# Performance work log

Measured on AMD Instinct MI355X. Metric: run time of the kernel, lower is better.

## Reference

```python
import math
import jax, jax.numpy as jnp
import numpy as np

B, T, D = 2, 2048, 1024
NUM_HEADS = 16
NUM_KV_HEADS = 4
HEAD_DIM = 64
ROPE_THETA = 500000.0


def precompute_freqs_cis(dim, seq_len, theta):
    freqs = 1.0 / theta ** (jnp.arange(0, dim, 2).astype(jnp.float32) / dim)
    freqs = jnp.outer(jnp.arange(seq_len), freqs)  # [T, dim//2]
    return jnp.cos(freqs), jnp.sin(freqs)


def apply_rotary_emb(xq, xk, cos, sin):
    # xq:[B,T,H,Dh], cos/sin:[T,Dh//2] -> broadcast as [1,T,1,Dh//2]
    c = cos[None, :, None, :]
    s = sin[None, :, None, :]

    def rot(x):
        xr = x.reshape(*x.shape[:-1], -1, 2)
        x0, x1 = xr[..., 0], xr[..., 1]
        return jnp.stack([x0 * c - x1 * s, x1 * c + x0 * s], axis=-1).reshape(x.shape)

    return rot(xq), rot(xk)


def setup_inputs() -> dict:
    key = jax.random.key(0)
    ks = jax.random.split(key, 5)
    x = jax.random.normal(ks[0], (B, T, D), dtype=jnp.float32)
    # causal mask [B,1,T,T]
    mask = jnp.broadcast_to(jnp.tril(jnp.ones((T, T), dtype=bool))[None, None], (B, 1, T, T))
    sq = 1.0 / math.sqrt(D)
    Wq = jax.random.normal(ks[1], (D, NUM_HEADS * HEAD_DIM), dtype=jnp.float32) * sq
    Wk = jax.random.normal(ks[2], (D, NUM_KV_HEADS * HEAD_DIM), dtype=jnp.float32) * sq
    Wv = jax.random.normal(ks[3], (D, NUM_KV_HEADS * HEAD_DIM), dtype=jnp.float32) * sq
    Wo = jax.random.normal(ks[4], (NUM_HEADS * HEAD_DIM, D), dtype=jnp.float32) * (1.0 / math.sqrt(NUM_HEADS * HEAD_DIM))
    return {"x": x, "mask": mask, "Wq": Wq, "Wk": Wk, "Wv": Wv, "Wo": Wo}


def reference(x, mask, Wq, Wk, Wv, Wo):
    b, t, _ = x.shape
    n_rep = NUM_HEADS // NUM_KV_HEADS
    q = (x @ Wq).reshape(b, t, NUM_HEADS, HEAD_DIM)
    k = (x @ Wk).reshape(b, t, NUM_KV_HEADS, HEAD_DIM)
    v = (x @ Wv).reshape(b, t, NUM_KV_HEADS, HEAD_DIM)
    cos, sin = precompute_freqs_cis(HEAD_DIM, t, ROPE_THETA)
    q, k = apply_rotary_emb(q, k, cos, sin)
    k = jnp.repeat(k, n_rep, axis=2)
    v = jnp.repeat(v, n_rep, axis=2)
    q = q.transpose(0, 2, 1, 3)  # [B,H,T,Dh]
    k = k.transpose(0, 2, 1, 3)
    v = v.transpose(0, 2, 1, 3)
    scale = 1.0 / math.sqrt(HEAD_DIM)
    attn = jnp.einsum('bhqd,bhkd->bhqk', q, k) * scale
    attn = jnp.where(mask, attn, -1e9)
    attn = jax.nn.softmax(attn, axis=-1)
    out = jnp.einsum('bhqk,bhkd->bhqd', attn, v)
    out = out.transpose(0, 2, 1, 3).reshape(b, t, -1)
    return out @ Wo
```

## Files before the change

kernel.cpp:

```cpp
#include <hip/hip_runtime.h>
#include <hip/hip_bf16.h>

#define B_  2
#define T_  2048
#define D_  1024
#define H_  16
#define KH_ 4
#define DH_ 64

typedef __attribute__((ext_vector_type(8))) short bf16x8;
typedef __attribute__((ext_vector_type(4))) float f32x4;

#define QSCALE 0.18033688011112043f

#if defined(__has_builtin)
#  if __has_builtin(__builtin_amdgcn_exp2f)
#    define EXP2F(x) __builtin_amdgcn_exp2f(x)
#  endif
#endif
#ifndef EXP2F
#  define EXP2F(x) exp2f(x)
#endif

__device__ __forceinline__ unsigned short f2bf(float f) {
  union { float f; unsigned int u; } v; v.f = f;
  return (unsigned short)((v.u + 0x7FFFu + ((v.u >> 16) & 1u)) >> 16);
}
__device__ __forceinline__ unsigned int pk2(float a, float b) {
  union { __hip_bfloat162 h2; unsigned int u; } v;
  v.h2 = __float22bfloat162_rn(make_float2(a, b));
  return v.u;
}

__device__ __forceinline__ void g2l16(const void* g, void* l) {
  __builtin_amdgcn_global_load_lds(
      (const __attribute__((address_space(1))) void*)g,
      (__attribute__((address_space(3))) void*)l, 16, 0, 0);
}


__global__ __launch_bounds__(256) void prep_kernel(
    const float* __restrict__ x,  const float* __restrict__ Wq,
    const float* __restrict__ Wk, const float* __restrict__ Wv,
    const float* __restrict__ Wo,
    short* __restrict__ xb, short* __restrict__ WT, short* __restrict__ WoT,
    float2* __restrict__ tbl) {
  __shared__ short Ts[64 * 72];
  const int bid = blockIdx.x, tid = threadIdx.x;

  if (bid < 2048) {
    const size_t i8 = ((size_t)bid * 256 + tid) * 8;
    const float4 a = *(const float4*)&x[i8];
    const float4 b = *(const float4*)&x[i8 + 4];
    uint4 p; p.x = pk2(a.x, a.y); p.y = pk2(a.z, a.w);
    p.z = pk2(b.x, b.y); p.w = pk2(b.z, b.w);
    *(uint4*)&xb[i8] = p;
  } else if (bid < 2688) {
    const bool isW = bid < 2432;
    const int idx = isW ? (bid - 2048) : (bid - 2432);
    const int n0 = (idx >> 4) * 64, k0 = (idx & 15) * 64;
    const float* src; int ncols, c0; short* dst;
    if (isW) {
      dst = WT;
      if (n0 < 1024)      { src = Wq; ncols = 1024; c0 = n0; }
      else if (n0 < 1280) { src = Wk; ncols = 256;  c0 = n0 - 1024; }
      else                { src = Wv; ncols = 256;  c0 = n0 - 1280; }
    } else { dst = WoT; src = Wo; ncols = 1024; c0 = n0; }
    for (int i = tid; i < 1024; i += 256) {
      const int kr = i >> 4, c4 = (i & 15) << 2;
      const int kc = isW ? kr : ((kr & 15) * 4 + (kr >> 4));
      const float4 w = *(const float4*)&src[(size_t)(k0 + kr) * ncols + c0 + c4];
      Ts[(c4 + 0) * 72 + kc] = (short)f2bf(w.x);
      Ts[(c4 + 1) * 72 + kc] = (short)f2bf(w.y);
      Ts[(c4 + 2) * 72 + kc] = (short)f2bf(w.z);
      Ts[(c4 + 3) * 72 + kc] = (short)f2bf(w.w);
    }
    __syncthreads();
    for (int c = tid; c < 512; c += 256) {
      const int nr = c >> 3, c8 = (c & 7) * 8;
      *(bf16x8*)&dst[(size_t)(n0 + nr) * 1024 + k0 + c8] =
          *(const bf16x8*)&Ts[nr * 72 + c8];
    }
  } else {
    const int e = (bid - 2688) * 256 + tid;
    const int t = e >> 5, i2 = e & 31;
    const float freq = exp2f(-(float)(2 * i2) * (18.931568569324174f / 64.0f));
    float sn, cs; sincosf((float)t * freq, &sn, &cs);
    tbl[e] = make_float2(cs, sn);
  }
}

__global__ __launch_bounds__(256) void qkv_mfma_kernel(
    const short* __restrict__ xb, const short* __restrict__ WT,
    const float2* __restrict__ tbl,
    short* __restrict__ qo, short* __restrict__ ko, short* __restrict__ vt) {
  __shared__ short Xsh[2][128 * 64];
  __shared__ short Wth[2][64 * 64];
  const int tid = threadIdx.x;
  const int lane = tid & 63, w = tid >> 6;
  const int lm = lane & 15, quad = lane >> 4;
  const int bid = blockIdx.x;
  const int xcd = bid & 7, slot = bid >> 3;
  const int m0 = (xcd * 4 + (slot & 3)) * 128;
  const int n0 = (slot >> 2) * 64;

  f32x4 acc[2][4];
  #pragma unroll
  for (int sm = 0; sm < 2; ++sm)
    #pragma unroll
    for (int ct = 0; ct < 4; ++ct) acc[sm][ct] = (f32x4){0.f, 0.f, 0.f, 0.f};

  auto stage = [&](int kt, int bsel) {
    #pragma unroll
    for (int u = 0; u < 4; ++u) {
      const int r = u * 32 + w * 8 + (lane >> 3);
      const int sb = (lane & 7) ^ (r & 7);
      g2l16(&xb[(size_t)(m0 + r) * 1024 + kt * 64 + sb * 8],
            &Xsh[bsel][(u * 32 + w * 8) * 64]);
    }
    #pragma unroll
    for (int u = 0; u < 2; ++u) {
      const int r = u * 32 + w * 8 + (lane >> 3);
      const int sb = (lane & 7) ^ (r & 7);
      g2l16(&WT[(size_t)(n0 + r) * 1024 + kt * 64 + sb * 8],
            &Wth[bsel][(u * 32 + w * 8) * 64]);
    }
  };

  stage(0, 0);
  for (int kt = 0; kt < 16; ++kt) {
    const int bsel = kt & 1;
    if (kt < 15) {
      stage(kt + 1, bsel ^ 1);
      asm volatile("s_waitcnt vmcnt(6)" ::: "memory");
    } else {
      asm volatile("s_waitcnt vmcnt(0)" ::: "memory");
    }
    __builtin_amdgcn_s_barrier();
    __builtin_amdgcn_sched_barrier(0);
    #pragma unroll
    for (int s2 = 0; s2 < 2; ++s2) {
      bf16x8 bfr[4];
      #pragma unroll
      for (int ct = 0; ct < 4; ++ct)
        bfr[ct] = *(const bf16x8*)&Wth[bsel][(ct * 16 + lm) * 64 +
                                            (((s2 * 4 + quad) ^ (lm & 7)) << 3)];
      #pragma unroll
      for (int sm = 0; sm < 2; ++sm) {
        const bf16x8 a = *(const bf16x8*)&Xsh[bsel][(w * 32 + sm * 16 + lm) * 64 +
                                            (((s2 * 4 + quad) ^ (lm & 7)) << 3)];
        #pragma unroll
        for (int ct = 0; ct < 4; ++ct)
          acc[sm][ct] =
              __builtin_amdgcn_mfma_f32_16x16x32_bf16(a, bfr[ct], acc[sm][ct], 0, 0, 0);
      }
    }
    __builtin_amdgcn_sched_barrier(0);
    __builtin_amdgcn_s_barrier();
  }

  if (n0 < 1280) {
    const bool isQ = n0 < 1024;
    short* outp = isQ ? qo : ko;
    const int base = isQ ? n0 : n0 - 1024;
    const int nh = isQ ? H_ : KH_;
    const int hh = base >> 6;
    const float post = isQ ? QSCALE : 1.0f;
    #pragma unroll
    for (int sm = 0; sm < 2; ++sm)
      #pragma unroll
      for (int r = 0; r < 4; ++r) {
        const int row = m0 + w * 32 + sm * 16 + quad * 4 + r;
        const int b = row >> 11, t = row & 2047;
        float v4[4];
        #pragma unroll
        for (int ct = 0; ct < 4; ++ct) {
          float val = acc[sm][ct][r];
          const float other = __shfl_xor(val, 1);
          const int ci = ct * 16 + lm;
          const float2 cs = tbl[t * 32 + (ci >> 1)];
          val = ((ci & 1) == 0) ? (val * cs.x - other * cs.y)
                                : (val * cs.x + other * cs.y);
          v4[ct] = val * post;
        }
        uint2 st; st.x = pk2(v4[0], v4[1]); st.y = pk2(v4[2], v4[3]);
        *(uint2*)&outp[((size_t)(b * nh + hh) * T_ + t) * DH_ + lm * 4] = st;
      }
  } else {
    short* XsF = &Xsh[0][0];
    __syncthreads();
    #pragma unroll
    for (int sm = 0; sm < 2; ++sm)
      #pragma unroll
      for (int r = 0; r < 4; ++r)
        #pragma unroll
        for (int ct = 0; ct < 4; ++ct)
          XsF[(w * 32 + sm * 16 + quad * 4 + r) * 72 + ct * 16 + lm] =
              (short)f2bf(acc[sm][ct][r]);
    __syncthreads();
    const int kh = (n0 - 1280) >> 6;
    const int b = m0 >> 11, t0 = m0 & 2047;
    short* vb = vt + (size_t)(b * KH_ + kh) * DH_ * T_;
    for (int c = tid; c < 1024; c += 256) {
      const int d = c >> 4, c8 = (c & 15) * 8;
      short tmp[8];
      #pragma unroll
      for (int j = 0; j < 8; ++j) {
        const int s = c8 + j, sg = s & 63;
        const int tok = (s & 64) | (sg & 35) | (((sg >> 2) & 1) << 4) |
                        (((sg >> 3) & 3) << 2);
        tmp[j] = XsF[tok * 72 + d];
      }
      *(bf16x8*)&vb[(size_t)d * T_ + t0 + c8] = *(bf16x8*)tmp;
    }
  }
}

__global__ __launch_bounds__(256, 4) void attn_mfma_kernel(
    const short* __restrict__ q, const short* __restrict__ k,
    const short* __restrict__ vt, short* __restrict__ att) {
  __shared__ short Ks[128 * 72];
  __shared__ short Vts[64 * 136];

  const int bx = blockIdx.x;
  const int jj = bx & 255, c2 = bx >> 8;
  int qt = (c2 & 1) ? (jj >> 3) : (31 - (jj >> 3));
  const int hb = (jj & 7) | (c2 << 3);
  const int h = hb >> 1, b = hb & 1;
  const int kh = h >> 2;
  const int tid = threadIdx.x;
  const int lane = tid & 63, w = tid >> 6;
  const int lm = lane & 15, quad = lane >> 4;
  const int q0 = qt * 64;

  const short* qb = q + (size_t)(b * H_ + h) * T_ * DH_;
  const short* kb = k + (size_t)(b * KH_ + kh) * T_ * DH_;
  const short* vb = vt + (size_t)(b * KH_ + kh) * DH_ * T_;

  bf16x8 ones;
  #pragma unroll
  for (int i = 0; i < 8; ++i) ones[i] = (short)0x3F80;

  bf16x8 aq[2];
  #pragma unroll
  for (int s = 0; s < 2; ++s)
    aq[s] = *(const bf16x8*)&qb[(size_t)(q0 + w * 16 + lm) * 64 + s * 32 + quad * 8];

  bf16x8 pk[4], pv[4];
  #pragma unroll
  for (int u = 0; u < 4; ++u) {
    const int c = tid + u * 256;
    const int row = c >> 3, c8 = (c & 7) * 8;
    pk[u] = *(const bf16x8*)&kb[(size_t)row * 64 + c8];
    const int d = c >> 4, c16 = (c & 15) * 8;
    pv[u] = *(const bf16x8*)&vb[(size_t)d * T_ + c16];
  }

  f32x4 oacc[4], lacc;
  #pragma unroll
  for (int i = 0; i < 4; ++i) oacc[i] = (f32x4){0.f, 0.f, 0.f, 0.f};
  lacc = (f32x4){0.f, 0.f, 0.f, 0.f};

  auto step = [&](int j, bool diag) {
    f32x4 sacc[4];
    #pragma unroll
    for (int i = 0; i < 4; ++i) sacc[i] = (f32x4){0.f, 0.f, 0.f, 0.f};
    __builtin_amdgcn_s_setprio(1);
    #pragma unroll
    for (int s2 = 0; s2 < 2; ++s2) {
      #pragma unroll
      for (int ct = 0; ct < 4; ++ct) {
        if (diag && ct > w) continue;
        const bf16x8 bb =
            *(const bf16x8*)&Ks[(j * 64 + ct * 16 + lm) * 72 + s2 * 32 + quad * 8];
        sacc[ct] = __builtin_amdgcn_mfma_f32_16x16x32_bf16(bb, aq[s2], sacc[ct], 0, 0, 0);
      }
    }
    __builtin_amdgcn_s_setprio(0);
    unsigned int pd[4][2];
    #pragma unroll
    for (int ct = 0; ct < 4; ++ct) {
      float p[4];
      #pragma unroll
      for (int r = 0; r < 4; ++r) {
        float e;
        if (diag && ct > w) e = 0.f;
        else {
          e = EXP2F(sacc[ct][r]);
          if (diag && ct == w && (quad * 4 + r) > lm) e = 0.f;
        }
        p[r] = e;
      }
      pd[ct][0] = pk2(p[0], p[1]);
      pd[ct][1] = pk2(p[2], p[3]);
    }
    __builtin_amdgcn_s_setprio(1);
    #pragma unroll
    for (int s2 = 0; s2 < 2; ++s2) {
      if (diag && 2 * s2 > w) continue;
      union { bf16x8 v; unsigned int u[4]; } pa;
      pa.u[0] = pd[2 * s2][0];     pa.u[1] = pd[2 * s2][1];
      pa.u[2] = pd[2 * s2 + 1][0]; pa.u[3] = pd[2 * s2 + 1][1];
      lacc = __builtin_amdgcn_mfma_f32_16x16x32_bf16(pa.v, ones, lacc, 0, 0, 0);
      #pragma unroll
      for (int ct = 0; ct < 4; ++ct) {
        const bf16x8 vfr = *(const bf16x8*)&Vts[(ct * 16 + lm) * 136 +
                                                j * 64 + s2 * 32 + quad * 8];
        oacc[ct] = __builtin_amdgcn_mfma_f32_16x16x32_bf16(pa.v, vfr, oacc[ct], 0, 0, 0);
      }
    }
    __builtin_amdgcn_s_setprio(0);
  };

  auto stage = [&](int r2) {
    __syncthreads();
    #pragma unroll
    for (int u = 0; u < 4; ++u) {
      const int c = tid + u * 256;
      const int row = c >> 3, c8 = (c & 7) * 8;
      *(bf16x8*)&Ks[row * 72 + c8] = pk[u];
      const int d = c >> 4, c16 = (c & 15) * 8;
      *(bf16x8*)&Vts[d * 136 + c16] = pv[u];
    }
    __syncthreads();
    const int r2n = (r2 + 2 <= qt) ? (r2 + 2) : r2;
    #pragma unroll
    for (int u = 0; u < 4; ++u) {
      const int c = tid + u * 256;
      const int row = c >> 3, c8 = (c & 7) * 8;
      pk[u] = *(const bf16x8*)&kb[(size_t)(r2n * 64 + row) * 64 + c8];
      const int d = c >> 4, c16 = (c & 15) * 8;
      pv[u] = *(const bf16x8*)&vb[(size_t)d * T_ + r2n * 64 + c16];
    }
  };

  int r2 = 0;
  for (; r2 + 1 <= qt; r2 += 2) {
    stage(r2);
    step(0, false);
    step(1, r2 + 1 == qt);
  }
  if (r2 == qt) {
    stage(r2);
    step(0, true);
  }

  #pragma unroll
  for (int r = 0; r < 4; ++r) {
    const int qrow = q0 + w * 16 + quad * 4 + r;
    const float inv = 1.f / lacc[r];
    uint2 st;
    st.x = pk2(oacc[0][r] * inv, oacc[1][r] * inv);
    st.y = pk2(oacc[2][r] * inv, oacc[3][r] * inv);
    *(uint2*)&att[((size_t)b * T_ + qrow) * 1024 + h * 64 + lm * 4] = st;
  }
}

__global__ __launch_bounds__(256) void outproj_mfma_kernel(
    const short* __restrict__ att, const short* __restrict__ WoT,
    float* __restrict__ out) {
  __shared__ short Xsh[2][128 * 64];
  __shared__ short Wth[2][64 * 64];
  const int tid = threadIdx.x;
  const int lane = tid & 63, w = tid >> 6;
  const int lm = lane & 15, quad = lane >> 4;
  const int bid = blockIdx.x;
  const int xcd = bid & 7, slot = bid >> 3;
  const int m0 = (xcd * 4 + (slot & 3)) * 128;
  const int n0 = (slot >> 2) * 64;

  f32x4 acc[2][4];
  #pragma unroll
  for (int sm = 0; sm < 2; ++sm)
    #pragma unroll
    for (int ct = 0; ct < 4; ++ct) acc[sm][ct] = (f32x4){0.f, 0.f, 0.f, 0.f};

  auto stage = [&](int kt, int bsel) {
    #pragma unroll
    for (int u = 0; u < 4; ++u) {
      const int r = u * 32 + w * 8 + (lane >> 3);
      const int sb = (lane & 7) ^ (r & 7);
      g2l16(&att[(size_t)(m0 + r) * 1024 + kt * 64 + sb * 8],
            &Xsh[bsel][(u * 32 + w * 8) * 64]);
    }
    #pragma unroll
    for (int u = 0; u < 2; ++u) {
      const int r = u * 32 + w * 8 + (lane >> 3);
      const int sb = (lane & 7) ^ (r & 7);
      g2l16(&WoT[(size_t)(n0 + r) * 1024 + kt * 64 + sb * 8],
            &Wth[bsel][(u * 32 + w * 8) * 64]);
    }
  };

  stage(0, 0);
  for (int kt = 0; kt < 16; ++kt) {
    const int bsel = kt & 1;
    if (kt < 15) {
      stage(kt + 1, bsel ^ 1);
      asm volatile("s_waitcnt vmcnt(6)" ::: "memory");
    } else {
      asm volatile("s_waitcnt vmcnt(0)" ::: "memory");
    }
    __builtin_amdgcn_s_barrier();
    __builtin_amdgcn_sched_barrier(0);
    #pragma unroll
    for (int s2 = 0; s2 < 2; ++s2) {
      bf16x8 bfr[4];
      #pragma unroll
      for (int ct = 0; ct < 4; ++ct)
        bfr[ct] = *(const bf16x8*)&Wth[bsel][(ct * 16 + lm) * 64 +
                                            (((s2 * 4 + quad) ^ (lm & 7)) << 3)];
      #pragma unroll
      for (int sm = 0; sm < 2; ++sm) {
        const bf16x8 a = *(const bf16x8*)&Xsh[bsel][(w * 32 + sm * 16 + lm) * 64 +
                                            (((s2 * 4 + quad) ^ (lm & 7)) << 3)];
        #pragma unroll
        for (int ct = 0; ct < 4; ++ct)
          acc[sm][ct] =
              __builtin_amdgcn_mfma_f32_16x16x32_bf16(a, bfr[ct], acc[sm][ct], 0, 0, 0);
      }
    }
    __builtin_amdgcn_sched_barrier(0);
    __builtin_amdgcn_s_barrier();
  }

  #pragma unroll
  for (int sm = 0; sm < 2; ++sm)
    #pragma unroll
    for (int r = 0; r < 4; ++r) {
      const int row = m0 + w * 32 + sm * 16 + quad * 4 + r;
      #pragma unroll
      for (int ct = 0; ct < 4; ++ct)
        out[(size_t)row * 1024 + n0 + ct * 16 + lm] = acc[sm][ct][r];
    }
}

extern "C" void kernel_launch(void* const* d_in, const int* in_sizes, int n_in,
                              void* d_out, int out_size, void* d_ws, size_t ws_size,
                              hipStream_t stream) {
  const float* x  = (const float*)d_in[0];
  const float* Wq = (const float*)d_in[2];
  const float* Wk = (const float*)d_in[3];
  const float* Wv = (const float*)d_in[4];
  const float* Wo = (const float*)d_in[5];
  float* out = (float*)d_out;

  short* xb   = (short*)d_ws;
  short* WT   = xb  + (size_t)4194304;
  short* WoT  = WT  + (size_t)1572864;
  short* qb   = WoT + (size_t)1048576;
  short* kb   = qb  + (size_t)4194304;
  short* vtb  = kb  + (size_t)1048576;
  short* attb = vtb + (size_t)1048576;
  float2* tbl = (float2*)(attb + (size_t)4194304);

  prep_kernel<<<dim3(2944), dim3(256), 0, stream>>>(
      x, Wq, Wk, Wv, Wo, xb, WT, WoT, tbl);
  qkv_mfma_kernel<<<dim3(768), dim3(256), 0, stream>>>(xb, WT, tbl, qb, kb, vtb);
  attn_mfma_kernel<<<dim3(1024), dim3(256), 0, stream>>>(qb, kb, vtb, attb);
  outproj_mfma_kernel<<<dim3(512), dim3(256), 0, stream>>>(attb, WoT, out);
}
```

Measured before the change: 169.4 us.

## Switch attention to 32x32x16 MFMA with 2x2 wave split and cross-wave reduction

Rewrites the attention inner loop to use 32x32x16 bf16 MFMA tiles. The four waves are split 2x2 over query rows and key columns, so each wave handles 32 queries by 32 keys, and partial outputs are reduced through shared memory at the end. The row sum is now accumulated in scalar registers instead of through a ones-matrix MFMA. The K/V LDS strides and the V/Wo column permutations are changed to match the new fragment layout. The intent is fewer MFMA issues and fewer LDS fragment loads per tile, at the cost of a final cross-wave reduction and extra synchronisation.

```diff
diff --git a/kernel.cpp b/kernel.cpp
--- a/kernel.cpp
+++ b/kernel.cpp
@@ -10,6 +10,7 @@
 
 typedef __attribute__((ext_vector_type(8))) short bf16x8;
 typedef __attribute__((ext_vector_type(4))) float f32x4;
+typedef __attribute__((ext_vector_type(16))) float f32x16;
 
 #define QSCALE 0.18033688011112043f
 
@@ -68,7 +69,7 @@
     } else { dst = WoT; src = Wo; ncols = 1024; c0 = n0; }
     for (int i = tid; i < 1024; i += 256) {
       const int kr = i >> 4, c4 = (i & 15) << 2;
-      const int kc = isW ? kr : ((kr & 15) * 4 + (kr >> 4));
+      const int kc = isW ? kr : ((kr & 31) * 2 + (kr >> 5));
       const float4 w = *(const float4*)&src[(size_t)(k0 + kr) * ncols + c0 + c4];
       Ts[(c4 + 0) * 72 + kc] = (short)f2bf(w.x);
       Ts[(c4 + 1) * 72 + kc] = (short)f2bf(w.y);
@@ -206,9 +207,9 @@
       short tmp[8];
       #pragma unroll
       for (int j = 0; j < 8; ++j) {
-        const int s = c8 + j, sg = s & 63;
-        const int tok = (s & 64) | (sg & 35) | (((sg >> 2) & 1) << 4) |
-                        (((sg >> 3) & 3) << 2);
+        const int s = c8 + j, p = s & 63;
+        const int tok = (s & 64) | (p & 51) | (((p >> 3) & 1) << 2) |
+                        (((p >> 2) & 1) << 3);
         tmp[j] = XsF[tok * 72 + d];
       }
       *(bf16x8*)&vb[(size_t)d * T_ + t0 + c8] = *(bf16x8*)tmp;
@@ -219,8 +220,9 @@
 __global__ __launch_bounds__(256, 4) void attn_mfma_kernel(
     const short* __restrict__ q, const short* __restrict__ k,
     const short* __restrict__ vt, short* __restrict__ att) {
-  __shared__ short Ks[128 * 72];
-  __shared__ short Vts[64 * 136];
+  __shared__ __align__(16) short SMEM[16768];
+  short* Ks = SMEM;
+  short* Vts = SMEM + 8448;
 
   const int bx = blockIdx.x;
   const int jj = bx & 255, c2 = bx >> 8;
@@ -230,21 +232,22 @@
   const int kh = h >> 2;
   const int tid = threadIdx.x;
   const int lane = tid & 63, w = tid >> 6;
-  const int lm = lane & 15, quad = lane >> 4;
+  const int wq = w >> 1, wk = w & 1;
+  const int l5 = lane & 31, hi = lane >> 5;
   const int q0 = qt * 64;
 
   const short* qb = q + (size_t)(b * H_ + h) * T_ * DH_;
   const short* kb = k + (size_t)(b * KH_ + kh) * T_ * DH_;
   const short* vb = vt + (size_t)(b * KH_ + kh) * DH_ * T_;
 
-  bf16x8 ones;
-  #pragma unroll
-  for (int i = 0; i < 8; ++i) ones[i] = (short)0x3F80;
-
-  bf16x8 aq[2];
-  #pragma unroll
-  for (int s = 0; s < 2; ++s)
-    aq[s] = *(const bf16x8*)&qb[(size_t)(q0 + w * 16 + lm) * 64 + s * 32 + quad * 8];
+  bf16x8 aq0, aq1, aq2, aq3;
+  {
+    const short* qr = &qb[(size_t)(q0 + wq * 32 + l5) * 64 + hi * 8];
+    aq0 = *(const bf16x8*)&qr[0];
+    aq1 = *(const bf16x8*)&qr[16];
+    aq2 = *(const bf16x8*)&qr[32];
+    aq3 = *(const bf16x8*)&qr[48];
+  }
 
   bf16x8 pk[4], pv[4];
   #pragma unroll
@@ -256,60 +259,55 @@
     pv[u] = *(const bf16x8*)&vb[(size_t)d * T_ + c16];
   }
 
-  f32x4 oacc[4], lacc;
+  f32x16 oacc0, oacc1;
   #pragma unroll
-  for (int i = 0; i < 4; ++i) oacc[i] = (f32x4){0.f, 0.f, 0.f, 0.f};
-  lacc = (f32x4){0.f, 0.f, 0.f, 0.f};
+  for (int i = 0; i < 16; ++i) { oacc0[i] = 0.f; oacc1[i] = 0.f; }
+  float lsum = 0.f;
 
   auto step = [&](int j, bool diag) {
-    f32x4 sacc[4];
-    #pragma unroll
-    for (int i = 0; i < 4; ++i) sacc[i] = (f32x4){0.f, 0.f, 0.f, 0.f};
-    __builtin_amdgcn_s_setprio(1);
-    #pragma unroll
-    for (int s2 = 0; s2 < 2; ++s2) {
-      #pragma unroll
-      for (int ct = 0; ct < 4; ++ct) {
-        if (diag && ct > w) continue;
-        const bf16x8 bb =
-            *(const bf16x8*)&Ks[(j * 64 + ct * 16 + lm) * 72 + s2 * 32 + quad * 8];
-        sacc[ct] = __builtin_amdgcn_mfma_f32_16x16x32_bf16(bb, aq[s2], sacc[ct], 0, 0, 0);
-      }
-    }
-    __builtin_amdgcn_s_setprio(0);
-    unsigned int pd[4][2];
-    #pragma unroll
-    for (int ct = 0; ct < 4; ++ct) {
-      float p[4];
-      #pragma unroll
-      for (int r = 0; r < 4; ++r) {
-        float e;
-        if (diag && ct > w) e = 0.f;
-        else {
-          e = EXP2F(sacc[ct][r]);
-          if (diag && ct == w && (quad * 4 + r) > lm) e = 0.f;
+    const bool skipall = diag && (wk > wq);
+    const bool dg = diag && (wk == wq);
+    f32x16 sacc;
+    #pragma unroll
+    for (int i = 0; i < 16; ++i) sacc[i] = 0.f;
+    if (!skipall) {
+      const short* kbase = &Ks[(j * 64 + wk * 32 + l5) * 66 + hi * 8];
+      __builtin_amdgcn_s_setprio(1);
+      sacc = __builtin_amdgcn_mfma_f32_32x32x16_bf16(*(const bf16x8*)&kbase[0],  aq0, sacc, 0, 0, 0);
+      sacc = __builtin_amdgcn_mfma_f32_32x32x16_bf16(*(const bf16x8*)&kbase[16], aq1, sacc, 0, 0, 0);
+      sacc = __builtin_amdgcn_mfma_f32_32x32x16_bf16(*(const bf16x8*)&kbase[32], aq2, sacc, 0, 0, 0);
+      sacc = __builtin_amdgcn_mfma_f32_32x32x16_bf16(*(const bf16x8*)&kbase[48], aq3, sacc, 0, 0, 0);
+      __builtin_amdgcn_s_setprio(0);
+    }
+    unsigned int pd[8];
+    #pragma unroll
+    for (int i = 0; i < 8; ++i) {
+      float e0 = 0.f, e1 = 0.f;
+      if (!skipall) {
+        const int r0 = 2 * i;
+        e0 = EXP2F(sacc[r0]);
+        e1 = EXP2F(sacc[r0 + 1]);
+        if (dg) {
+          const int k0 = (r0 & 3) + 8 * (r0 >> 2) + 4 * hi;
+          if (k0 > l5) e0 = 0.f;
+          if (k0 + 1 > l5) e1 = 0.f;
         }
-        p[r] = e;
-      }
-      pd[ct][0] = pk2(p[0], p[1]);
-      pd[ct][1] = pk2(p[2], p[3]);
-    }
-    __builtin_amdgcn_s_setprio(1);
-    #pragma unroll
-    for (int s2 = 0; s2 < 2; ++s2) {
-      if (diag && 2 * s2 > w) continue;
+      }
+      lsum += e0 + e1;
+      pd[i] = pk2(e0, e1);
+    }
+    if (!skipall) {
+      const short* vbase = &Vts[l5 * 130 + j * 64 + wk * 32 + hi * 8];
+      __builtin_amdgcn_s_setprio(1);
       union { bf16x8 v; unsigned int u[4]; } pa;
-      pa.u[0] = pd[2 * s2][0];     pa.u[1] = pd[2 * s2][1];
-      pa.u[2] = pd[2 * s2 + 1][0]; pa.u[3] = pd[2 * s2 + 1][1];
-      lacc = __builtin_amdgcn_mfma_f32_16x16x32_bf16(pa.v, ones, lacc, 0, 0, 0);
-      #pragma unroll
-      for (int ct = 0; ct < 4; ++ct) {
-        const bf16x8 vfr = *(const bf16x8*)&Vts[(ct * 16 + lm) * 136 +
-                                                j * 64 + s2 * 32 + quad * 8];
-        oacc[ct] = __builtin_amdgcn_mfma_f32_16x16x32_bf16(pa.v, vfr, oacc[ct], 0, 0, 0);
-      }
-    }
-    __builtin_amdgcn_s_setprio(0);
+      pa.u[0] = pd[0]; pa.u[1] = pd[1]; pa.u[2] = pd[2]; pa.u[3] = pd[3];
+      oacc0 = __builtin_amdgcn_mfma_f32_32x32x16_bf16(pa.v, *(const bf16x8*)&vbase[0],        oacc0, 0, 0, 0);
+      oacc1 = __builtin_amdgcn_mfma_f32_32x32x16_bf16(pa.v, *(const bf16x8*)&vbase[32 * 130], oacc1, 0, 0, 0);
+      pa.u[0] = pd[4]; pa.u[1] = pd[5]; pa.u[2] = pd[6]; pa.u[3] = pd[7];
+      oacc0 = __builtin_amdgcn_mfma_f32_32x32x16_bf16(pa.v, *(const bf16x8*)&vbase[16],            oacc0, 0, 0, 0);
+      oacc1 = __builtin_amdgcn_mfma_f32_32x32x16_bf16(pa.v, *(const bf16x8*)&vbase[32 * 130 + 16], oacc1, 0, 0, 0);
+      __builtin_amdgcn_s_setprio(0);
+    }
   };
 
   auto stage = [&](int r2) {
@@ -318,9 +316,9 @@
     for (int u = 0; u < 4; ++u) {
       const int c = tid + u * 256;
       const int row = c >> 3, c8 = (c & 7) * 8;
-      *(bf16x8*)&Ks[row * 72 + c8] = pk[u];
+      *(bf16x8*)&Ks[row * 66 + c8] = pk[u];
       const int d = c >> 4, c16 = (c & 15) * 8;
-      *(bf16x8*)&Vts[d * 136 + c16] = pv[u];
+      *(bf16x8*)&Vts[d * 130 + c16] = pv[u];
     }
     __syncthreads();
     const int r2n = (r2 + 2 <= qt) ? (r2 + 2) : r2;
@@ -345,14 +343,41 @@
     step(0, true);
   }
 
-  #pragma unroll
-  for (int r = 0; r < 4; ++r) {
-    const int qrow = q0 + w * 16 + quad * 4 + r;
-    const float inv = 1.f / lacc[r];
-    uint2 st;
-    st.x = pk2(oacc[0][r] * inv, oacc[1][r] * inv);
-    st.y = pk2(oacc[2][r] * inv, oacc[3][r] * inv);
-    *(uint2*)&att[((size_t)b * T_ + qrow) * 1024 + h * 64 + lm * 4] = st;
+  lsum += __shfl_xor(lsum, 32);
+  __syncthreads();
+  float* RED = (float*)SMEM;
+  float* LSQ = RED + 2 * 64 * 36;
+  LSQ[wk * 64 + wq * 32 + l5] = lsum;
+  const int base = (wq * 64 + lane) * 36;
+  if (wk == 1) {
+    #pragma unroll
+    for (int i = 0; i < 4; ++i) {
+      f32x4 t0 = {oacc0[4*i], oacc0[4*i+1], oacc0[4*i+2], oacc0[4*i+3]};
+      *(f32x4*)&RED[base + i * 4] = t0;
+      f32x4 t1 = {oacc1[4*i], oacc1[4*i+1], oacc1[4*i+2], oacc1[4*i+3]};
+      *(f32x4*)&RED[base + 16 + i * 4] = t1;
+    }
+  }
+  __syncthreads();
+  if (wk == 0) {
+    #pragma unroll
+    for (int i = 0; i < 4; ++i) {
+      const f32x4 t0 = *(const f32x4*)&RED[base + i * 4];
+      const f32x4 t1 = *(const f32x4*)&RED[base + 16 + i * 4];
+      #pragma unroll
+      for (int jx = 0; jx < 4; ++jx) {
+        oacc0[4*i + jx] += t0[jx];
+        oacc1[4*i + jx] += t1[jx];
+      }
+    }
+    #pragma unroll
+    for (int r = 0; r < 16; ++r) {
+      const int qr = (r & 3) + 8 * (r >> 2) + 4 * hi;
+      const float inv = 1.f / (LSQ[wq * 32 + qr] + LSQ[64 + wq * 32 + qr]);
+      const unsigned int pw = pk2(oacc0[r] * inv, oacc1[r] * inv);
+      *(unsigned int*)&att[((size_t)b * T_ + q0 + wq * 32 + qr) * 1024 +
+                           h * 64 + l5 * 2] = pw;
+    }
   }
 }
 
```

New measurement: 261.9 us. +54.6%, slower.
